# Kernel tuning notes

Measured on AMD Instinct MI355X. Metric: run time of the kernel, lower is better.

The kernel has to match this reference:

```python
import jax, jax.numpy as jnp
import numpy as np

N = 50000      # nodes
IN = 128       # in_dim
HID = 128      # hidden_dim
HEADS = 4
OUT = HID // HEADS   # per-head out_channels
R = 8          # num_relations
E = 640000     # message-passing edges
E2 = 200000    # decode edge pairs
NC = 8         # num_classes
EPS_LN = 1e-5


def layer_norm(x, g, b):
    m = x.mean(-1, keepdims=True)
    v = ((x - m) ** 2).mean(-1, keepdims=True)
    return (x - m) * jax.lax.rsqrt(v + EPS_LN) * g + b


def rgat_conv(x, edge_index, edge_type, W, q, k, b):
    # PyG RGATConv defaults: additive-self-attention, across-relation softmax,
    # concat=True, negative_slope=0.2, sum aggregation.
    src, dst = edge_index[0], edge_index[1]
    # relation-specific transform for all nodes, then gather per edge
    xw = jnp.einsum('ni,rio->nro', x, W)          # [N, R, HID]
    xi = xw[dst, edge_type]                        # [E, HID] target feats
    xj = xw[src, edge_type]                        # [E, HID] source feats
    alpha = jax.nn.leaky_relu(xi @ q + xj @ k, negative_slope=0.2)  # [E, HEADS]
    # softmax over incoming edges of each destination node (per head)
    amax = jax.ops.segment_max(alpha, dst, num_segments=N)
    amax = jnp.where(jnp.isfinite(amax), amax, 0.0)
    ex = jnp.exp(alpha - amax[dst])
    den = jax.ops.segment_sum(ex, dst, num_segments=N)
    attn = ex / (den[dst] + 1e-16)                 # [E, HEADS]
    msg = (xj.reshape(E, HEADS, OUT) * attn[:, :, None]).reshape(E, HID)
    out = jax.ops.segment_sum(msg, dst, num_segments=N)  # [N, HID]
    return out + b


def setup_inputs() -> dict:
    key = jax.random.key(0)
    ks = jax.random.split(key, 12)
    sI = 1.0 / np.sqrt(IN)
    sH = 1.0 / np.sqrt(HID)
    return {
        'x': jax.random.normal(ks[0], (N, IN), jnp.float32),
        'edge_index': jax.random.randint(ks[1], (2, E), 0, N),
        'edge_type': jax.random.randint(ks[2], (E,), 0, R),
        'edges': jax.random.randint(ks[3], (E2, 2), 0, N),
        'w1': jax.random.normal(ks[4], (R, IN, HID), jnp.float32) * sI,
        'q1': jax.random.normal(ks[5], (HID, HEADS), jnp.float32) * sH,
        'k1': jax.random.normal(ks[6], (HID, HEADS), jnp.float32) * sH,
        'b1': jnp.zeros((HID,), jnp.float32),
        'w2': jax.random.normal(ks[7], (R, HID, HID), jnp.float32) * sH,
        'q2': jax.random.normal(ks[8], (HID, HEADS), jnp.float32) * sH,
        'k2': jax.random.normal(ks[9], (HID, HEADS), jnp.float32) * sH,
        'b2': jnp.zeros((HID,), jnp.float32),
        'ln1_g': jnp.ones((HID,), jnp.float32),
        'ln1_b': jnp.zeros((HID,), jnp.float32),
        'ln2_g': jnp.ones((HID,), jnp.float32),
        'ln2_b': jnp.zeros((HID,), jnp.float32),
        'mw1': jax.random.normal(ks[10], (2 * HID, HID), jnp.float32) / np.sqrt(2 * HID),
        'mb1': jnp.zeros((HID,), jnp.float32),
        'mw2': jax.random.normal(ks[11], (HID, NC), jnp.float32) * sH,
        'mb2': jnp.zeros((NC,), jnp.float32),
    }


def reference(x, edge_index, edge_type, edges,
              w1, q1, k1, b1, w2, q2, k2, b2,
              ln1_g, ln1_b, ln2_g, ln2_b,
              mw1, mb1, mw2, mb2):
    # encode (dropout is identity in eval mode)
    h1 = rgat_conv(x, edge_index, edge_type, w1, q1, k1, b1)
    h1 = layer_norm(jax.nn.relu(h1), ln1_g, ln1_b)
    h2 = rgat_conv(h1, edge_index, edge_type, w2, q2, k2, b2)
    h2 = layer_norm(jax.nn.relu(h2), ln2_g, ln2_b)
    h = h1 + h2
    # decode: gather node pairs, concat, MLP
    z = jnp.concatenate([h[edges[:, 0]], h[edges[:, 1]]], axis=1)  # [E2, 2*HID]
    z = jax.nn.gelu(z @ mw1 + mb1, approximate=False)
    return z @ mw2 + mb2  # [E2, NC]
```

## Files before the change

kernel.cpp:

```cpp
#include <hip/hip_runtime.h>
#include <hip/hip_bf16.h>

#define NN    50000
#define RR    8
#define HIDC  128
#define NHEADS 4
#define EE    640000
#define EE2   200000
#define NCL   8

typedef __hip_bfloat16 bf16;
typedef unsigned short u16;
typedef __attribute__((ext_vector_type(8))) short short8;
typedef __attribute__((ext_vector_type(4))) float floatx4;

__device__ __forceinline__ float us2f(u16 u) {
    return __uint_as_float(((unsigned)u) << 16);
}
__device__ __forceinline__ float bf2f(bf16 v) { return __bfloat162float(v); }
__device__ __forceinline__ u16 f2us(float f) {
    bf16 h = __float2bfloat16(f);
    return *(u16*)&h;
}
__device__ __forceinline__ float ldf(const void* p, int i, bool f32) {
    return f32 ? ((const float*)p)[i] : us2f(((const u16*)p)[i]);
}

__global__ __launch_bounds__(1024) void k_sniff(const u16* __restrict__ x, int* __restrict__ flags) {
    __shared__ int cnt;
    if (threadIdx.x == 0) cnt = 0;
    __syncthreads();
    int c = 0;
#pragma unroll
    for (int it = 0; it < 8; it++) {
        ushort4 a = ((const ushort4*)x)[(it * 1024 + threadIdx.x) * 2];
        ushort4 b = ((const ushort4*)x)[(it * 1024 + threadIdx.x) * 2 + 1];
        c += (((a.x >> 7) & 0xFF) == 0xFF) + (((a.y >> 7) & 0xFF) == 0xFF)
           + (((a.z >> 7) & 0xFF) == 0xFF) + (((a.w >> 7) & 0xFF) == 0xFF)
           + (((b.x >> 7) & 0xFF) == 0xFF) + (((b.y >> 7) & 0xFF) == 0xFF)
           + (((b.z >> 7) & 0xFF) == 0xFF) + (((b.w >> 7) & 0xFF) == 0xFF);
    }
    c += __shfl_xor(c, 32); c += __shfl_xor(c, 16); c += __shfl_xor(c, 8);
    c += __shfl_xor(c, 4);  c += __shfl_xor(c, 2);  c += __shfl_xor(c, 1);
    if ((threadIdx.x & 63) == 0) atomicAdd(&cnt, c);
    __syncthreads();
    if (threadIdx.x == 0) { flags[0] = (cnt > 16) ? 1 : 0; flags[1] = 0; }
}

__global__ void k_zero(int* __restrict__ p, int n) {
    int i = blockIdx.x * 256 + threadIdx.x;
    if (i < n) p[i] = 0;
}
__global__ void k_hist(const int* __restrict__ ei, int* __restrict__ deg) {
    int e = blockIdx.x * 256 + threadIdx.x;
    if (e < EE) atomicAdd(&deg[ei[EE + e]], 1);
}
__global__ __launch_bounds__(256) void k_scan1(const int* __restrict__ deg,
                                               int* __restrict__ bsum) {
    int i = blockIdx.x * 256 + threadIdx.x;
    int v = (i < NN) ? deg[i] : 0;
    __shared__ int red[4];
    int lane = threadIdx.x & 63, w = threadIdx.x >> 6;
#pragma unroll
    for (int off = 32; off; off >>= 1) v += __shfl_xor(v, off);
    if (lane == 0) red[w] = v;
    __syncthreads();
    if (threadIdx.x == 0) bsum[blockIdx.x] = red[0] + red[1] + red[2] + red[3];
}
__global__ __launch_bounds__(256) void k_scan2(const int* __restrict__ bsum,
                                               int* __restrict__ boff,
                                               int* __restrict__ rowptr) {
    __shared__ int s[256];
    int t = threadIdx.x;
    s[t] = (t < 196) ? bsum[t] : 0;
    __syncthreads();
    for (int off = 1; off < 256; off <<= 1) {
        int u = (t >= off) ? s[t - off] : 0;
        __syncthreads();
        s[t] += u;
        __syncthreads();
    }
    if (t < 196) boff[t] = (t == 0) ? 0 : s[t - 1];
    if (t == 255) rowptr[NN] = s[255];
}
__global__ __launch_bounds__(256) void k_scan3(int* __restrict__ deg ,
                                               const int* __restrict__ boff,
                                               int* __restrict__ rowptr) {
    __shared__ int s[256];
    int t = threadIdx.x;
    int i = blockIdx.x * 256 + t;
    int v = (i < NN) ? deg[i] : 0;
    s[t] = v;
    __syncthreads();
    for (int off = 1; off < 256; off <<= 1) {
        int u = (t >= off) ? s[t - off] : 0;
        __syncthreads();
        s[t] += u;
        __syncthreads();
    }
    if (i < NN) {
        int val = boff[blockIdx.x] + s[t] - v;
        rowptr[i] = val;
        deg[i] = val;
    }
}
__global__ void k_scatter(const int* __restrict__ ei, const int* __restrict__ et,
                          int* __restrict__ cursor, int* __restrict__ elist) {
    int e = blockIdx.x * 256 + threadIdx.x;
    if (e >= EE) return;
    int pos = atomicAdd(&cursor[ei[EE + e]], 1);
    elist[pos] = ei[e] * RR + et[e];
}

__global__ void k_qkw(const void* __restrict__ w1, const void* __restrict__ w2,
                      const void* __restrict__ q1, const void* __restrict__ k1,
                      const void* __restrict__ q2, const void* __restrict__ k2,
                      float* __restrict__ qkw, const int* __restrict__ fl) {
    int idx = blockIdx.x * 256 + threadIdx.x;
    if (idx >= 16384) return;
    const bool f = fl[0] != 0;
    int mat = idx >> 10;
    int i   = (idx >> 3) & 127;
    int h8  = idx & 7;
    const void* W = (mat >= 8) ? w2 : w1;
    const void* qk = (mat >= 8) ? ((h8 < 4) ? q2 : k2) : ((h8 < 4) ? q1 : k1);
    int h = h8 & 3;
    int r = mat & 7;
    float acc = 0.f;
    for (int o = 0; o < HIDC; o++)
        acc += ldf(W, (r * HIDC + i) * HIDC + o, f) * ldf(qk, o * NHEADS + h, f);
    qkw[idx] = acc;
}

__global__ void k_wswz(const void* __restrict__ w1, const void* __restrict__ w2,
                       const float* __restrict__ qkw,
                       u16* __restrict__ Wf2, const int* __restrict__ fl) {
    int idx = blockIdx.x * 256 + threadIdx.x;
    if (idx >= 36864) return;
    const bool f = fl[0] != 0;
    int mat = idx / 2304, rest = idx % 2304;
    int c = rest >> 8, q = (rest >> 6) & 3, ln = rest & 63;
    int k0 = q * 32 + (ln >> 4) * 8;
    int nn = c * 16 + (ln & 15);
    int r = mat & 7;
    u16 o[8];
    if (c < 8) {
        const void* W = (mat >= 8) ? w2 : w1;
#pragma unroll
        for (int j = 0; j < 8; j++)
            o[j] = f2us(ldf(W, (r * HIDC + k0 + j) * HIDC + nn, f));
    } else {
        int col = nn - 128;
#pragma unroll
        for (int j = 0; j < 8; j++)
            o[j] = (col < 8) ? f2us(qkw[mat * 1024 + (k0 + j) * 8 + col]) : (u16)0;
    }
    u16* dst = Wf2 + (size_t)mat * 18432 + (size_t)(((c * 4 + q) * 64 + ln) * 8);
    *(ushort4*)dst       = ushort4{o[0], o[1], o[2], o[3]};
    *(ushort4*)(dst + 4) = ushort4{o[4], o[5], o[6], o[7]};
}

__global__ __launch_bounds__(512) void k_xw2(const void* __restrict__ X,
                                             const u16* __restrict__ Wf2,
                                             bf16* __restrict__ xw,
                                             float* __restrict__ sbuf,
                                             float* __restrict__ tbuf,
                                             const int* __restrict__ fx,
                                             int layer) {
    __shared__ u16 Xs[64 * 136];
    __shared__ u16 Os[8][16 * 136];
    const int tid = threadIdx.x;
    const int n0 = blockIdx.x * 64;
    const bool xf = fx[0] != 0;
    for (int v = tid; v < 2048; v += 512) {
        int row = v >> 5, c4 = (v & 31) * 4, n = n0 + row;
        ushort4 o = {0, 0, 0, 0};
        if (n < NN) {
            if (xf) {
                float4 hv = *(const float4*)((const float*)X + (size_t)n * HIDC + c4);
                o = ushort4{f2us(hv.x), f2us(hv.y), f2us(hv.z), f2us(hv.w)};
            } else {
                o = *(const ushort4*)((const u16*)X + (size_t)n * HIDC + c4);
            }
        }
        *(ushort4*)&Xs[row * 136 + c4] = o;
    }
    __syncthreads();
    const int w = tid >> 6, lane = tid & 63;
    const int wr = w & 3;
    const int rh = w >> 2;
    short8 af[4];
#pragma unroll
    for (int q = 0; q < 4; q++)
        af[q] = *(const short8*)&Xs[(16 * wr + (lane & 15)) * 136 + q * 32 + (lane >> 4) * 8];
    u16* Ow = Os[w];
    for (int rr = 0; rr < 4; rr++) {
        const int r = rh * 4 + rr;
        const u16* Wfr = Wf2 + (size_t)(layer * 8 + r) * 18432;
#pragma unroll
        for (int c = 0; c < 9; c++) {
            floatx4 acc = {0.f, 0.f, 0.f, 0.f};
#pragma unroll
            for (int q = 0; q < 4; q++) {
                short8 bfr = *(const short8*)&Wfr[(size_t)(((c * 4 + q) * 64 + lane) * 8)];
                acc = __builtin_amdgcn_mfma_f32_16x16x32_bf16(af[q], bfr, acc, 0, 0, 0);
            }
            if (c < 8) {
                int col = c * 16 + (lane & 15);
#pragma unroll
                for (int reg = 0; reg < 4; reg++) {
                    int lp = (lane >> 4) * 4 + reg;
                    Ow[lp * 136 + col] = f2us(acc[reg]);
                }
            } else {
                int cl = lane & 15;
                if (cl < 8) {
                    float* dstp = (cl < 4) ? sbuf : tbuf;
                    int h = cl & 3;
#pragma unroll
                    for (int reg = 0; reg < 4; reg++) {
                        int p = 16 * wr + (lane >> 4) * 4 + reg;
                        int n = n0 + p;
                        if (n < NN) dstp[(size_t)(n * RR + r) * 4 + h] = acc[reg];
                    }
                }
            }
        }
#pragma unroll
        for (int i = 0; i < 4; i++) {
            int v = i * 64 + lane;
            int lrow = v >> 4;
            int c8 = (v & 15) * 8;
            int n = n0 + 16 * wr + lrow;
            if (n < NN) {
                short8 hv = *(const short8*)&Ow[lrow * 136 + c8];
                *(short8*)((u16*)xw + (size_t)(n * RR + r) * HIDC + c8) = hv;
            }
        }
    }
}

__global__ __launch_bounds__(256) void k_attn(const int* __restrict__ rowptr,
                                              const int* __restrict__ srlist,
                                              const float* __restrict__ sb,
                                              const float* __restrict__ tb,
                                              const bf16* __restrict__ xw,
                                              const void* __restrict__ b,
                                              const void* __restrict__ g,
                                              const void* __restrict__ bb,
                                              const u16* __restrict__ hprev,
                                              u16* __restrict__ hout,
                                              const int* __restrict__ fl) {
    __shared__ int   srs[16][16];
    __shared__ float exs[16][17][4];
    const int tid = threadIdx.x;
    const int grp = tid >> 4;
    const int sl  = tid & 15;
    const int hh  = sl >> 2;
    const int d   = blockIdx.x * 16 + grp;
    const bool f = fl[0] != 0;
    const int start = rowptr[d], end = rowptr[d + 1];
    float m0 = -1e30f, m1 = -1e30f, m2 = -1e30f, m3 = -1e30f;
    float l0 = 0.f, l1 = 0.f, l2 = 0.f, l3 = 0.f;
    float acc[8];
#pragma unroll
    for (int i = 0; i < 8; i++) acc[i] = 0.f;
    for (int c0 = start; c0 < end; c0 += 16) {
        int n = end - c0;
        if (n > 16) n = 16;
        float a0, a1, a2, a3;
        int sr = 0;
        if (sl < n) {
            sr = srlist[c0 + sl];
            int r = sr & 7;
            float4 si = *(const float4*)&sb[(size_t)(d * RR + r) * 4];
            float4 tj = *(const float4*)&tb[(size_t)sr * 4];
            a0 = si.x + tj.x; a0 = a0 >= 0.f ? a0 : 0.2f * a0;
            a1 = si.y + tj.y; a1 = a1 >= 0.f ? a1 : 0.2f * a1;
            a2 = si.z + tj.z; a2 = a2 >= 0.f ? a2 : 0.2f * a2;
            a3 = si.w + tj.w; a3 = a3 >= 0.f ? a3 : 0.2f * a3;
        } else { a0 = a1 = a2 = a3 = -1e30f; }
        float c0m = a0, c1m = a1, c2m = a2, c3m = a3;
#pragma unroll
        for (int off = 8; off; off >>= 1) {
            c0m = fmaxf(c0m, __shfl_xor(c0m, off));
            c1m = fmaxf(c1m, __shfl_xor(c1m, off));
            c2m = fmaxf(c2m, __shfl_xor(c2m, off));
            c3m = fmaxf(c3m, __shfl_xor(c3m, off));
        }
        float n0 = fmaxf(m0, c0m), n1 = fmaxf(m1, c1m);
        float n2 = fmaxf(m2, c2m), n3 = fmaxf(m3, c3m);
        float s0 = __expf(m0 - n0), s1 = __expf(m1 - n1);
        float s2 = __expf(m2 - n2), s3 = __expf(m3 - n3);
        float e0 = __expf(a0 - n0), e1 = __expf(a1 - n1);
        float e2 = __expf(a2 - n2), e3 = __expf(a3 - n3);
        float t0 = e0, t1 = e1, t2 = e2, t3 = e3;
#pragma unroll
        for (int off = 8; off; off >>= 1) {
            t0 += __shfl_xor(t0, off);
            t1 += __shfl_xor(t1, off);
            t2 += __shfl_xor(t2, off);
            t3 += __shfl_xor(t3, off);
        }
        l0 = l0 * s0 + t0; l1 = l1 * s1 + t1;
        l2 = l2 * s2 + t2; l3 = l3 * s3 + t3;
        srs[grp][sl] = sr;
        *(float4*)&exs[grp][sl][0] = float4{e0, e1, e2, e3};
        float scl = hh == 0 ? s0 : hh == 1 ? s1 : hh == 2 ? s2 : s3;
#pragma unroll
        for (int i = 0; i < 8; i++) acc[i] *= scl;
        int j = 0;
        while (j + 8 <= n) {
            short8 u[8]; float wv[8];
#pragma unroll
            for (int t = 0; t < 8; t++) {
                int s = srs[grp][j + t];
                wv[t] = exs[grp][j + t][hh];
                u[t] = *(const short8*)((const u16*)xw + (size_t)s * HIDC + sl * 8);
            }
#pragma unroll
            for (int t = 0; t < 8; t++)
#pragma unroll
                for (int i = 0; i < 8; i++) acc[i] += wv[t] * us2f((u16)u[t][i]);
            j += 8;
        }
        if (j + 4 <= n) {
            short8 u[4]; float wv[4];
#pragma unroll
            for (int t = 0; t < 4; t++) {
                int s = srs[grp][j + t];
                wv[t] = exs[grp][j + t][hh];
                u[t] = *(const short8*)((const u16*)xw + (size_t)s * HIDC + sl * 8);
            }
#pragma unroll
            for (int t = 0; t < 4; t++)
#pragma unroll
                for (int i = 0; i < 8; i++) acc[i] += wv[t] * us2f((u16)u[t][i]);
            j += 4;
        }
        if (j + 2 <= n) {
            short8 u[2]; float wv[2];
#pragma unroll
            for (int t = 0; t < 2; t++) {
                int s = srs[grp][j + t];
                wv[t] = exs[grp][j + t][hh];
                u[t] = *(const short8*)((const u16*)xw + (size_t)s * HIDC + sl * 8);
            }
#pragma unroll
            for (int t = 0; t < 2; t++)
#pragma unroll
                for (int i = 0; i < 8; i++) acc[i] += wv[t] * us2f((u16)u[t][i]);
            j += 2;
        }
        if (j < n) {
            int s = srs[grp][j];
            float wv = exs[grp][j][hh];
            short8 u = *(const short8*)((const u16*)xw + (size_t)s * HIDC + sl * 8);
#pragma unroll
            for (int i = 0; i < 8; i++) acc[i] += wv * us2f((u16)u[i]);
        }
        m0 = n0; m1 = n1; m2 = n2; m3 = n3;
    }
    float ld = hh == 0 ? l0 : hh == 1 ? l1 : hh == 2 ? l2 : l3;
    float inv = 1.f / (ld + 1e-16f);
    float v[8];
#pragma unroll
    for (int i = 0; i < 8; i++)
        v[i] = fmaxf(acc[i] * inv + ldf(b, sl * 8 + i, f), 0.f);
    float sum = 0.f;
#pragma unroll
    for (int i = 0; i < 8; i++) sum += v[i];
#pragma unroll
    for (int off = 8; off; off >>= 1) sum += __shfl_xor(sum, off);
    float mean = sum * (1.f / 128.f);
    float sq = 0.f;
#pragma unroll
    for (int i = 0; i < 8; i++) { v[i] -= mean; sq += v[i] * v[i]; }
#pragma unroll
    for (int off = 8; off; off >>= 1) sq += __shfl_xor(sq, off);
    float rstd = rsqrtf(sq * (1.f / 128.f) + 1e-5f);
    short8 o;
#pragma unroll
    for (int i = 0; i < 8; i++) {
        float y = v[i] * rstd * ldf(g, sl * 8 + i, f) + ldf(bb, sl * 8 + i, f);
        o[i] = (short)f2us(y);
    }
    if (hprev) {
        short8 hv = *(const short8*)&hprev[(size_t)d * HIDC + sl * 8];
#pragma unroll
        for (int i = 0; i < 8; i++)
            o[i] = (short)f2us(us2f((u16)o[i]) + us2f((u16)hv[i]));
    }
    *(short8*)&hout[(size_t)d * HIDC + sl * 8] = o;
}

__global__ void k_dswz(const void* __restrict__ mw1, const void* __restrict__ mw2,
                       u16* __restrict__ Wf, const int* __restrict__ fl) {
    int idx = blockIdx.x * 256 + threadIdx.x;
    if (idx >= 4352) return;
    const bool f = fl[0] != 0;
    u16 o[8];
    if (idx < 4096) {
        int c = idx >> 9, q = (idx >> 6) & 7, ln = idx & 63;
        int k0 = q * 32 + (ln >> 4) * 8;
        int nn = c * 16 + (ln & 15);
#pragma unroll
        for (int j = 0; j < 8; j++)
            o[j] = f2us(ldf(mw1, (k0 + j) * HIDC + nn, f));
    } else {
        int fidx = idx - 4096;
        int q = fidx >> 6, ln = fidx & 63;
        int k0 = q * 32 + (ln >> 4) * 8;
        int nn = ln & 15;
#pragma unroll
        for (int j = 0; j < 8; j++)
            o[j] = (nn < 8) ? f2us(ldf(mw2, (k0 + j) * NCL + nn, f)) : (u16)0;
    }
    *(ushort4*)&Wf[idx * 8]     = ushort4{o[0], o[1], o[2], o[3]};
    *(ushort4*)&Wf[idx * 8 + 4] = ushort4{o[4], o[5], o[6], o[7]};
}

__global__ __launch_bounds__(256) void k_decode2(const u16* __restrict__ h,
                                                 const int* __restrict__ edges,
                                                 const u16* __restrict__ Wf,
                                                 const void* __restrict__ mb1,
                                                 const void* __restrict__ mb2,
                                                 void* __restrict__ out,
                                                 const int* __restrict__ fl) {
    __shared__ u16 zsu[64 * 136];
    const int tid = threadIdx.x;
    const bool f = fl[0] != 0;
    const int p0 = blockIdx.x * 64;
    const int w = tid >> 6, lane = tid & 63;
    const int m = 16 * w + (lane & 15);
    const int g = lane >> 4;
    const int na = edges[(size_t)(p0 + m) * 2];
    const int nb = edges[(size_t)(p0 + m) * 2 + 1];
    short8 af[8];
#pragma unroll
    for (int q = 0; q < 8; q++) {
        int k0 = q * 32 + g * 8;
        af[q] = *(const short8*)(h + (size_t)((k0 >> 7) ? nb : na) * HIDC + (k0 & 127));
    }
#pragma unroll
    for (int c = 0; c < 8; c++) {
        floatx4 acc = {0.f, 0.f, 0.f, 0.f};
#pragma unroll
        for (int q = 0; q < 8; q++) {
            short8 bfr = *(const short8*)&Wf[(size_t)(((c * 8 + q) * 64 + lane) * 8)];
            acc = __builtin_amdgcn_mfma_f32_16x16x32_bf16(af[q], bfr, acc, 0, 0, 0);
        }
        int col = c * 16 + (lane & 15);
        float bv = ldf(mb1, col, f);
#pragma unroll
        for (int reg = 0; reg < 4; reg++) {
            int p = 16 * w + (lane >> 4) * 4 + reg;
            float z = acc[reg] + bv;
            zsu[p * 136 + col] = f2us(0.5f * z * (1.f + erff(z * 0.70710678118654752f)));
        }
    }
    floatx4 acc2 = {0.f, 0.f, 0.f, 0.f};
#pragma unroll
    for (int q = 0; q < 4; q++) {
        short8 af2 = *(const short8*)&zsu[m * 136 + q * 32 + g * 8];
        short8 bfr2 = *(const short8*)&Wf[32768 + (size_t)((q * 64 + lane) * 8)];
        acc2 = __builtin_amdgcn_mfma_f32_16x16x32_bf16(af2, bfr2, acc2, 0, 0, 0);
    }
    int col16 = lane & 15;
    if (col16 < 8) {
        float bv2 = ldf(mb2, col16, f);
#pragma unroll
        for (int reg = 0; reg < 4; reg++) {
            int p = 16 * w + (lane >> 4) * 4 + reg;
            float sv = acc2[reg] + bv2;
            size_t oi = (size_t)(p0 + p) * NCL + col16;
            if (f) ((float*)out)[oi] = sv;
            else   ((bf16*)out)[oi] = __float2bfloat16(sv);
        }
    }
}

extern "C" void kernel_launch(void* const* d_in, const int* in_sizes, int n_in,
                              void* d_out, int out_size, void* d_ws, size_t ws_size,
                              hipStream_t stream) {
    (void)in_sizes; (void)n_in; (void)out_size; (void)ws_size;
    const void* x    = d_in[0];
    const int* ei    = (const int*)d_in[1];
    const int* et    = (const int*)d_in[2];
    const int* edges = (const int*)d_in[3];
    const void* w1 = d_in[4];
    const void* q1 = d_in[5];
    const void* k1 = d_in[6];
    const void* b1 = d_in[7];
    const void* w2 = d_in[8];
    const void* q2 = d_in[9];
    const void* k2 = d_in[10];
    const void* b2 = d_in[11];
    const void* ln1g = d_in[12];
    const void* ln1b = d_in[13];
    const void* ln2g = d_in[14];
    const void* ln2b = d_in[15];
    const void* mw1 = d_in[16];
    const void* mb1 = d_in[17];
    const void* mw2 = d_in[18];
    const void* mb2 = d_in[19];

    char* ws = (char*)d_ws;
    bf16* xwb   = (bf16*)ws;
    u16* Wf     = (u16*)ws;
    float* sbuf = (float*)(ws + 102400000);
    float* tbuf = (float*)(ws + 108800000);
    u16* h1     = (u16*)(ws + 115200000);
    u16* hsum   = (u16*)(ws + 140800000);
    u16* Wf2    = (u16*)(ws + 153600000);
    int* rowptr = (int*)(ws + 166400000);
    int* cursor = (int*)(ws + 166600016);
    int* elist  = (int*)(ws + 166800016);
    float* qkw  = (float*)(ws + 169360016);
    int* bsum   = (int*)qkw;
    int* boff   = bsum + 256;
    int* flags  = (int*)(ws + 169425552);

    k_sniff<<<1, 1024, 0, stream>>>((const u16*)x, flags);

    k_zero<<<196, 256, 0, stream>>>(cursor, NN);
    k_hist<<<2500, 256, 0, stream>>>(ei, cursor);
    k_scan1<<<196, 256, 0, stream>>>(cursor, bsum);
    k_scan2<<<1, 256, 0, stream>>>(bsum, boff, rowptr);
    k_scan3<<<196, 256, 0, stream>>>(cursor, boff, rowptr);
    k_scatter<<<2500, 256, 0, stream>>>(ei, et, cursor, elist);
    k_qkw<<<64, 256, 0, stream>>>(w1, w2, q1, k1, q2, k2, qkw, flags);
    k_wswz<<<144, 256, 0, stream>>>(w1, w2, qkw, Wf2, flags);

    for (int layer = 0; layer < 2; ++layer) {
        const void* b  = layer ? b2 : b1;
        const void* lg = layer ? ln2g : ln1g;
        const void* lb = layer ? ln2b : ln1b;
        k_xw2<<<782, 512, 0, stream>>>(layer ? (const void*)h1 : x, Wf2, xwb,
                                       sbuf, tbuf,
                                       layer ? flags + 1 : flags, layer);
        k_attn<<<3125, 256, 0, stream>>>(rowptr, elist, sbuf, tbuf, xwb,
                                         b, lg, lb,
                                         layer ? h1 : (const u16*)nullptr,
                                         layer ? hsum : h1, flags);
    }
    k_dswz<<<17, 256, 0, stream>>>(mw1, mw2, Wf, flags);
    k_decode2<<<3125, 256, 0, stream>>>(hsum, edges, Wf, mb1, mb2, d_out, flags);
}
```

Before: 482.1 us.

## Split attention into separate score-softmax and aggregation kernels

The fused online-softmax attention kernel becomes two kernels. k_score computes leaky-relu scores and exp weights per edge into a buffer, plus inverse denominators per node and head. k_agg then does a fixed 8- or 16-wide weighted gather of the bf16 source features. This removes the per-chunk rescaling and the 8/4/2/1 tail branches from the gather loop, giving it fuller unrolled loads. The cost is an extra launch per layer, about 10 MB of edge weights written and read back, and wasted zero-weight loads of row 0 when a chunk has fewer than 8 or 16 edges.

New measurement: 482.6 us. No clear change (+0.1%).

```diff
diff --git a/kernel.cpp b/kernel.cpp
--- a/kernel.cpp
+++ b/kernel.cpp
@@ -240,17 +240,117 @@
     }
 }
 
-__global__ __launch_bounds__(256) void k_attn(const int* __restrict__ rowptr,
-                                              const int* __restrict__ srlist,
-                                              const float* __restrict__ sb,
-                                              const float* __restrict__ tb,
-                                              const bf16* __restrict__ xw,
-                                              const void* __restrict__ b,
-                                              const void* __restrict__ g,
-                                              const void* __restrict__ bb,
-                                              const u16* __restrict__ hprev,
-                                              u16* __restrict__ hout,
-                                              const int* __restrict__ fl) {
+__global__ __launch_bounds__(256) void k_score(const int* __restrict__ rowptr,
+                                               const int* __restrict__ srlist,
+                                               const float* __restrict__ sb,
+                                               const float* __restrict__ tb,
+                                               float* __restrict__ abuf,
+                                               float* __restrict__ linv) {
+    __shared__ float sbs[16][8][4];
+    const int tid = threadIdx.x;
+    const int grp = tid >> 4, sl = tid & 15;
+    const int d = blockIdx.x * 16 + grp;
+    const int start = rowptr[d], end = rowptr[d + 1];
+    if (sl < 8)
+        *(float4*)&sbs[grp][sl][0] = *(const float4*)&sb[(size_t)(d * RR + sl) * 4];
+    const int nE = end - start;
+    float m0 = -1e30f, m1 = -1e30f, m2 = -1e30f, m3 = -1e30f;
+    float l0 = 0.f, l1 = 0.f, l2 = 0.f, l3 = 0.f;
+    if (nE <= 16) {
+        float a0, a1, a2, a3;
+        if (sl < nE) {
+            int sr = srlist[start + sl];
+            int r = sr & 7;
+            float4 tj = *(const float4*)&tb[(size_t)sr * 4];
+            a0 = sbs[grp][r][0] + tj.x; a0 = a0 >= 0.f ? a0 : 0.2f * a0;
+            a1 = sbs[grp][r][1] + tj.y; a1 = a1 >= 0.f ? a1 : 0.2f * a1;
+            a2 = sbs[grp][r][2] + tj.z; a2 = a2 >= 0.f ? a2 : 0.2f * a2;
+            a3 = sbs[grp][r][3] + tj.w; a3 = a3 >= 0.f ? a3 : 0.2f * a3;
+        } else { a0 = a1 = a2 = a3 = -1e30f; }
+        float c0m = a0, c1m = a1, c2m = a2, c3m = a3;
+#pragma unroll
+        for (int off = 8; off; off >>= 1) {
+            c0m = fmaxf(c0m, __shfl_xor(c0m, off));
+            c1m = fmaxf(c1m, __shfl_xor(c1m, off));
+            c2m = fmaxf(c2m, __shfl_xor(c2m, off));
+            c3m = fmaxf(c3m, __shfl_xor(c3m, off));
+        }
+        m0 = fmaxf(c0m, -1e30f); m1 = c1m; m2 = c2m; m3 = c3m;
+        float e0 = 0.f, e1 = 0.f, e2 = 0.f, e3 = 0.f;
+        if (sl < nE) {
+            e0 = __expf(a0 - m0); e1 = __expf(a1 - m1);
+            e2 = __expf(a2 - m2); e3 = __expf(a3 - m3);
+            *(float4*)&abuf[(size_t)(start + sl) * 4] = float4{e0, e1, e2, e3};
+        }
+        l0 = e0; l1 = e1; l2 = e2; l3 = e3;
+#pragma unroll
+        for (int off = 8; off; off >>= 1) {
+            l0 += __shfl_xor(l0, off);
+            l1 += __shfl_xor(l1, off);
+            l2 += __shfl_xor(l2, off);
+            l3 += __shfl_xor(l3, off);
+        }
+    } else {
+        for (int c0 = start; c0 < end; c0 += 16) {
+            int n = end - c0; if (n > 16) n = 16;
+            float a0, a1, a2, a3;
+            if (sl < n) {
+                int sr = srlist[c0 + sl];
+                int r = sr & 7;
+                float4 tj = *(const float4*)&tb[(size_t)sr * 4];
+                a0 = sbs[grp][r][0] + tj.x; a0 = a0 >= 0.f ? a0 : 0.2f * a0;
+                a1 = sbs[grp][r][1] + tj.y; a1 = a1 >= 0.f ? a1 : 0.2f * a1;
+                a2 = sbs[grp][r][2] + tj.z; a2 = a2 >= 0.f ? a2 : 0.2f * a2;
+                a3 = sbs[grp][r][3] + tj.w; a3 = a3 >= 0.f ? a3 : 0.2f * a3;
+                *(float4*)&abuf[(size_t)(c0 + sl) * 4] = float4{a0, a1, a2, a3};
+            } else { a0 = a1 = a2 = a3 = -1e30f; }
+            m0 = fmaxf(m0, a0); m1 = fmaxf(m1, a1);
+            m2 = fmaxf(m2, a2); m3 = fmaxf(m3, a3);
+        }
+#pragma unroll
+        for (int off = 8; off; off >>= 1) {
+            m0 = fmaxf(m0, __shfl_xor(m0, off));
+            m1 = fmaxf(m1, __shfl_xor(m1, off));
+            m2 = fmaxf(m2, __shfl_xor(m2, off));
+            m3 = fmaxf(m3, __shfl_xor(m3, off));
+        }
+        for (int c0 = start; c0 < end; c0 += 16) {
+            int n = end - c0; if (n > 16) n = 16;
+            float e0 = 0.f, e1 = 0.f, e2 = 0.f, e3 = 0.f;
+            if (sl < n) {
+                float4 a = *(const float4*)&abuf[(size_t)(c0 + sl) * 4];
+                e0 = __expf(a.x - m0); e1 = __expf(a.y - m1);
+                e2 = __expf(a.z - m2); e3 = __expf(a.w - m3);
+                *(float4*)&abuf[(size_t)(c0 + sl) * 4] = float4{e0, e1, e2, e3};
+            }
+            l0 += e0; l1 += e1; l2 += e2; l3 += e3;
+        }
+#pragma unroll
+        for (int off = 8; off; off >>= 1) {
+            l0 += __shfl_xor(l0, off);
+            l1 += __shfl_xor(l1, off);
+            l2 += __shfl_xor(l2, off);
+            l3 += __shfl_xor(l3, off);
+        }
+    }
+    if (sl == 0) {
+        *(float4*)&linv[(size_t)d * 4] =
+            float4{1.f / (l0 + 1e-16f), 1.f / (l1 + 1e-16f),
+                   1.f / (l2 + 1e-16f), 1.f / (l3 + 1e-16f)};
+    }
+}
+
+__global__ __launch_bounds__(256) void k_agg(const int* __restrict__ rowptr,
+                                             const int* __restrict__ srlist,
+                                             const float* __restrict__ abuf,
+                                             const float* __restrict__ linvb,
+                                             const bf16* __restrict__ xw,
+                                             const void* __restrict__ b,
+                                             const void* __restrict__ g,
+                                             const void* __restrict__ bb,
+                                             const u16* __restrict__ hprev,
+                                             u16* __restrict__ hout,
+                                             const int* __restrict__ fl) {
     __shared__ int   srs[16][16];
     __shared__ float exs[16][17][4];
     const int tid = threadIdx.x;
@@ -260,109 +360,48 @@
     const int d   = blockIdx.x * 16 + grp;
     const bool f = fl[0] != 0;
     const int start = rowptr[d], end = rowptr[d + 1];
-    float m0 = -1e30f, m1 = -1e30f, m2 = -1e30f, m3 = -1e30f;
-    float l0 = 0.f, l1 = 0.f, l2 = 0.f, l3 = 0.f;
     float acc[8];
 #pragma unroll
     for (int i = 0; i < 8; i++) acc[i] = 0.f;
     for (int c0 = start; c0 < end; c0 += 16) {
         int n = end - c0;
         if (n > 16) n = 16;
-        float a0, a1, a2, a3;
         int sr = 0;
+        float4 e4 = {0.f, 0.f, 0.f, 0.f};
         if (sl < n) {
             sr = srlist[c0 + sl];
-            int r = sr & 7;
-            float4 si = *(const float4*)&sb[(size_t)(d * RR + r) * 4];
-            float4 tj = *(const float4*)&tb[(size_t)sr * 4];
-            a0 = si.x + tj.x; a0 = a0 >= 0.f ? a0 : 0.2f * a0;
-            a1 = si.y + tj.y; a1 = a1 >= 0.f ? a1 : 0.2f * a1;
-            a2 = si.z + tj.z; a2 = a2 >= 0.f ? a2 : 0.2f * a2;
-            a3 = si.w + tj.w; a3 = a3 >= 0.f ? a3 : 0.2f * a3;
-        } else { a0 = a1 = a2 = a3 = -1e30f; }
-        float c0m = a0, c1m = a1, c2m = a2, c3m = a3;
-#pragma unroll
-        for (int off = 8; off; off >>= 1) {
-            c0m = fmaxf(c0m, __shfl_xor(c0m, off));
-            c1m = fmaxf(c1m, __shfl_xor(c1m, off));
-            c2m = fmaxf(c2m, __shfl_xor(c2m, off));
-            c3m = fmaxf(c3m, __shfl_xor(c3m, off));
-        }
-        float n0 = fmaxf(m0, c0m), n1 = fmaxf(m1, c1m);
-        float n2 = fmaxf(m2, c2m), n3 = fmaxf(m3, c3m);
-        float s0 = __expf(m0 - n0), s1 = __expf(m1 - n1);
-        float s2 = __expf(m2 - n2), s3 = __expf(m3 - n3);
-        float e0 = __expf(a0 - n0), e1 = __expf(a1 - n1);
-        float e2 = __expf(a2 - n2), e3 = __expf(a3 - n3);
-        float t0 = e0, t1 = e1, t2 = e2, t3 = e3;
-#pragma unroll
-        for (int off = 8; off; off >>= 1) {
-            t0 += __shfl_xor(t0, off);
-            t1 += __shfl_xor(t1, off);
-            t2 += __shfl_xor(t2, off);
-            t3 += __shfl_xor(t3, off);
-        }
-        l0 = l0 * s0 + t0; l1 = l1 * s1 + t1;
-        l2 = l2 * s2 + t2; l3 = l3 * s3 + t3;
+            e4 = *(const float4*)&abuf[(size_t)(c0 + sl) * 4];
+        }
         srs[grp][sl] = sr;
-        *(float4*)&exs[grp][sl][0] = float4{e0, e1, e2, e3};
-        float scl = hh == 0 ? s0 : hh == 1 ? s1 : hh == 2 ? s2 : s3;
-#pragma unroll
-        for (int i = 0; i < 8; i++) acc[i] *= scl;
-        int j = 0;
-        while (j + 8 <= n) {
+        *(float4*)&exs[grp][sl][0] = e4;
+        {
             short8 u[8]; float wv[8];
 #pragma unroll
             for (int t = 0; t < 8; t++) {
-                int s = srs[grp][j + t];
-                wv[t] = exs[grp][j + t][hh];
+                int s = srs[grp][t];
+                wv[t] = exs[grp][t][hh];
                 u[t] = *(const short8*)((const u16*)xw + (size_t)s * HIDC + sl * 8);
             }
 #pragma unroll
             for (int t = 0; t < 8; t++)
 #pragma unroll
                 for (int i = 0; i < 8; i++) acc[i] += wv[t] * us2f((u16)u[t][i]);
-            j += 8;
-        }
-        if (j + 4 <= n) {
-            short8 u[4]; float wv[4];
-#pragma unroll
-            for (int t = 0; t < 4; t++) {
-                int s = srs[grp][j + t];
-                wv[t] = exs[grp][j + t][hh];
+        }
+        if (n > 8) {
+            short8 u[8]; float wv[8];
+#pragma unroll
+            for (int t = 0; t < 8; t++) {
+                int s = srs[grp][8 + t];
+                wv[t] = exs[grp][8 + t][hh];
                 u[t] = *(const short8*)((const u16*)xw + (size_t)s * HIDC + sl * 8);
             }
 #pragma unroll
-            for (int t = 0; t < 4; t++)
+            for (int t = 0; t < 8; t++)
 #pragma unroll
                 for (int i = 0; i < 8; i++) acc[i] += wv[t] * us2f((u16)u[t][i]);
-            j += 4;
-        }
-        if (j + 2 <= n) {
-            short8 u[2]; float wv[2];
-#pragma unroll
-            for (int t = 0; t < 2; t++) {
-                int s = srs[grp][j + t];
-                wv[t] = exs[grp][j + t][hh];
-                u[t] = *(const short8*)((const u16*)xw + (size_t)s * HIDC + sl * 8);
-            }
-#pragma unroll
-            for (int t = 0; t < 2; t++)
-#pragma unroll
-                for (int i = 0; i < 8; i++) acc[i] += wv[t] * us2f((u16)u[t][i]);
-            j += 2;
-        }
-        if (j < n) {
-            int s = srs[grp][j];
-            float wv = exs[grp][j][hh];
-            short8 u = *(const short8*)((const u16*)xw + (size_t)s * HIDC + sl * 8);
-#pragma unroll
-            for (int i = 0; i < 8; i++) acc[i] += wv * us2f((u16)u[i]);
-        }
-        m0 = n0; m1 = n1; m2 = n2; m3 = n3;
-    }
-    float ld = hh == 0 ? l0 : hh == 1 ? l1 : hh == 2 ? l2 : l3;
-    float inv = 1.f / (ld + 1e-16f);
+        }
+    }
+    float inv = linvb[(size_t)d * 4 + hh];
     float v[8];
 #pragma unroll
     for (int i = 0; i < 8; i++)
@@ -511,6 +550,8 @@
     float* sbuf = (float*)(ws + 102400000);
     float* tbuf = (float*)(ws + 108800000);
     u16* h1     = (u16*)(ws + 115200000);
+    float* abuf = (float*)(ws + 128000000);
+    float* linv = (float*)(ws + 138240000);
     u16* hsum   = (u16*)(ws + 140800000);
     u16* Wf2    = (u16*)(ws + 153600000);
     int* rowptr = (int*)(ws + 166400000);
@@ -539,10 +580,11 @@
         k_xw2<<<782, 512, 0, stream>>>(layer ? (const void*)h1 : x, Wf2, xwb,
                                        sbuf, tbuf,
                                        layer ? flags + 1 : flags, layer);
-        k_attn<<<3125, 256, 0, stream>>>(rowptr, elist, sbuf, tbuf, xwb,
-                                         b, lg, lb,
-                                         layer ? h1 : (const u16*)nullptr,
-                                         layer ? hsum : h1, flags);
+        k_score<<<3125, 256, 0, stream>>>(rowptr, elist, sbuf, tbuf, abuf, linv);
+        k_agg<<<3125, 256, 0, stream>>>(rowptr, elist, abuf, linv, xwb,
+                                        b, lg, lb,
+                                        layer ? h1 : (const u16*)nullptr,
+                                        layer ? hsum : h1, flags);
     }
     k_dswz<<<17, 256, 0, stream>>>(mw1, mw2, Wf, flags);
     k_decode2<<<3125, 256, 0, stream>>>(hsum, edges, Wf, mb1, mb2, d_out, flags);
```
